# Optimization experiments

Measured on AMD Instinct MI355X. Metric: run time of the kernel, lower is better.

The kernel has to match this reference:

```python
import jax, jax.numpy as jnp
import numpy as np

# plan steps: (downsample_factor, bins_min, bins_max)
PLAN = [(2, 10, 14), (4, 16, 20)]


def _downsample(x, scale):
    # F.interpolate(mode='linear', align_corners=False, scale_factor=1/scale)
    in_len = x.shape[-1]
    out_len = in_len // scale
    sf = in_len / out_len
    src = jnp.maximum((jnp.arange(out_len, dtype=jnp.float32) + 0.5) * sf - 0.5, 0.0)
    i0 = jnp.floor(src).astype(jnp.int32)
    w = src - i0
    i1 = jnp.minimum(i0 + 1, in_len - 1)
    return x[..., i0] * (1.0 - w) + x[..., i1] * w


def _groupshiftadd(x, g):
    # one FFA butterfly stage with group size g
    B, C, R, nc = x.shape
    xg = x.reshape(B, C, R // g, g, nc)
    i = np.arange(g)
    iA = i // 2
    iB = iA + g // 2
    Bs = (i + 1) // 2
    # roll(v, Bs): y[j] = v[(j - Bs) mod nc]; static gather indices
    col = (np.arange(nc)[None, :] - Bs[:, None]) % nc  # (g, nc)
    a = xg[:, :, :, iA, :]                     # (B,C,G,g,nc)
    b = xg[:, :, :, iB[:, None], col]          # (B,C,G,g,nc) shifted rows
    return (a + b).reshape(B, C, R, nc)


def _forward(x):
    std_dev = jnp.std(x, axis=2, ddof=1)  # torch .std(2) is unbiased
    outs = []
    for ds, bmin, bmax in PLAN:
        down = _downsample(x, ds)
        L = down.shape[-1]
        for bins in range(bmin, bmax):
            trunc = L % bins
            arr = down[:, :, :L - trunc] if trunc else down
            r = arr.reshape(arr.shape[0], arr.shape[1], -1, bins)
            ini_rows = r.shape[2]
            k = int(np.ceil(np.log2(ini_rows)))
            target_rows = 2 ** k
            add = target_rows - ini_rows
            if add:
                pad = jnp.zeros((r.shape[0], r.shape[1], add, bins), r.dtype)
                r = jnp.concatenate([r, pad], axis=2)
            y = r
            for stage in range(1, k + 1):
                y = _groupshiftadd(y, 2 ** stage)
            mx = y.max(axis=3)
            # torch.median returns lower middle element for even sizes
            med = jnp.sort(y, axis=3)[..., (bins - 1) // 2]
            snr = (mx - med) / std_dev[:, :, None] / np.sqrt(float(ini_rows))
            outs.append(snr)  # (B, C, target_rows)
    return jnp.concatenate(outs, axis=2)


def setup_inputs() -> dict:
    key = jax.random.key(0)
    x = jax.random.normal(key, (8, 4, 262144), dtype=jnp.float32)
    return {"x": x}


def reference(x):
    return _forward(x)
```

## Files before the change

### kernel.cpp

```cpp
#include <hip/hip_runtime.h>
#include <cmath>


constexpr int NSEQ    = 32;
constexpr int NLEN    = 262144;
constexpr int OUTROWS = 81920;
constexpr int STDCH   = 32;

constexpr int cilog2(int v) { int r = 0; while (v > 1) { v >>= 1; ++r; } return r; }

constexpr size_t SCROFF[8] = {0, 6291456, 12582912, 18874368,
                              27262976, 29360128, 31981568, 34603008};

__device__ __forceinline__ unsigned bf16rne(float f) {
    unsigned u = __float_as_uint(f);
    return (u + 0x7FFFu + ((u >> 16) & 1u)) >> 16;
}
__device__ __forceinline__ unsigned pk2(float lo, float hi) {
    return bf16rne(lo) | (bf16rne(hi) << 16);
}

__global__ __launch_bounds__(256)
void std_partial(const float* __restrict__ x, float2* __restrict__ part)
{
    const int seq = blockIdx.x, ch = blockIdx.y;
    constexpr int N4 = NLEN / 4 / STDCH;
    const float4* xp = reinterpret_cast<const float4*>(x + (size_t)seq * NLEN) + (size_t)ch * N4;
    float s = 0.f, s2 = 0.f;
    for (int i = threadIdx.x; i < N4; i += 256) {
        float4 v = xp[i];
        s  += (v.x + v.y) + (v.z + v.w);
        s2 += (v.x * v.x + v.y * v.y) + (v.z * v.z + v.w * v.w);
    }
    #pragma unroll
    for (int off = 32; off > 0; off >>= 1) {
        s  += __shfl_down(s, off, 64);
        s2 += __shfl_down(s2, off, 64);
    }
    __shared__ float2 ws[4];
    const int w = threadIdx.x >> 6, l = threadIdx.x & 63;
    if (l == 0) ws[w] = make_float2(s, s2);
    __syncthreads();
    if (threadIdx.x == 0) {
        float a = ws[0].x + ws[1].x + ws[2].x + ws[3].x;
        float b = ws[0].y + ws[1].y + ws[2].y + ws[3].y;
        part[seq * STDCH + ch] = make_float2(a, b);
    }
}

template<int DS, int BINS, int K, int S0, int CPAD>
__device__ __forceinline__
void passA_body(float* __restrict__ buf, const float* __restrict__ xs,
                unsigned short* __restrict__ scrC, int R, int blk, int sl)
{
    constexpr int G      = 1 << S0;
    constexpr int M      = 1 << (K - S0);
    constexpr int PAIRS  = G / 2;
    constexpr int CSPLIT = 512 / PAIRS;
    constexpr int H      = (BINS + CSPLIT - 1) / CSPLIT;
    const int t = threadIdx.x;
    float* b0 = buf;
    float* b1 = buf + BINS * G;

    const int fmax = max(0, min(G * BINS, R * BINS - blk * G * BINS));

    if constexpr (DS == 2) {
        const float4* src4 = reinterpret_cast<const float4*>(xs + 2 * (size_t)blk * G * BINS);
        constexpr int NF4 = G * BINS / 2;
        for (int i = t; i < NF4; i += 512) {
            const int f0 = 2 * i;
            if (f0 < fmax) {
                float4 v = src4[i];
                int lr = f0 / BINS, c = f0 - lr * BINS;
                b0[c * G + lr] = 0.5f * (v.x + v.y);
                if (f0 + 1 < fmax) {
                    int c1 = c + 1, lr1 = lr;
                    if (c1 == BINS) { c1 = 0; ++lr1; }
                    b0[c1 * G + lr1] = 0.5f * (v.z + v.w);
                }
            }
        }
    } else {
        const float4* src4 = reinterpret_cast<const float4*>(xs + 4 * (size_t)blk * G * BINS);
        constexpr int NF4 = G * BINS;
        for (int i = t; i < NF4; i += 512) {
            if (i < fmax) {
                float4 v = src4[i];
                int lr = i / BINS, c = i - lr * BINS;
                b0[c * G + lr] = 0.5f * (v.y + v.z);
            }
        }
    }
    for (int f = fmax + t; f < G * BINS; f += 512) {
        int lr = f / BINS, c = f - lr * BINS;
        b0[c * G + lr] = 0.f;
    }
    __syncthreads();

    const int pr  = t & (PAIRS - 1);
    const int chi = t / PAIRS;
    const int c0  = chi * H;
    for (int s = 1; s <= S0; ++s) {
        const float* src = (s & 1) ? b0 : b1;
        float*       dst = (s & 1) ? b1 : b0;
        const int half    = 1 << (s - 1);
        const int qp      = pr & (half - 1);
        const int grpbase = (pr >> (s - 1)) << s;
        const int rA = grpbase + qp, rB = rA + half, ro = grpbase + 2 * qp;
        const int shift = qp % BINS;
        int sc = c0 - shift; if (sc < 0) sc += BINS;
        int scm1 = sc - 1;   if (scm1 < 0) scm1 += BINS;
        float bprev = src[scm1 * G + rB];
        #pragma unroll
        for (int i2 = 0; i2 < H; ++i2) {
            const int c = c0 + i2;
            if (c < BINS) {
                float a  = src[c * G + rA];
                float bc = src[sc * G + rB];
                float2 o; o.x = a + bc; o.y = a + bprev;
                *reinterpret_cast<float2*>(&dst[c * G + ro]) = o;
                bprev = bc;
                ++sc; if (sc == BINS) sc = 0;
            }
        }
        __syncthreads();
    }

    const float* fin = (S0 & 1) ? b1 : b0;
    if constexpr (G == 512) {
        const int lr = t;
        unsigned u[CPAD / 2];
        #pragma unroll
        for (int k = 0; k < CPAD / 2; ++k) {
            const int ca = 2 * k, cb = 2 * k + 1;
            float fa = (ca < BINS) ? fin[ca * G + lr] : 0.f;
            float fb = (cb < BINS) ? fin[cb * G + lr] : 0.f;
            u[k] = pk2(fa, fb);
        }
        unsigned short* dst = scrC + ((size_t)(sl * M + blk) * G + lr) * CPAD;
        if constexpr (CPAD == 12) {
            uint2* d2 = reinterpret_cast<uint2*>(dst);
            d2[0] = make_uint2(u[0], u[1]);
            d2[1] = make_uint2(u[2], u[3]);
            d2[2] = make_uint2(u[4], u[5]);
        } else {
            uint4* d4 = reinterpret_cast<uint4*>(dst);
            d4[0] = make_uint4(u[0], u[1], u[2], u[3]);
            d4[1] = make_uint4(u[4], u[5], u[6], u[7]);
        }
    } else {
        const int lr = t & 255, chh = t >> 8;
        constexpr int CH = CPAD / 2;
        unsigned u[CH / 2];
        #pragma unroll
        for (int k = 0; k < CH / 2; ++k) {
            const int ca = chh * CH + 2 * k, cb = ca + 1;
            float fa = (ca < BINS) ? fin[ca * G + lr] : 0.f;
            float fb = (cb < BINS) ? fin[cb * G + lr] : 0.f;
            u[k] = pk2(fa, fb);
        }
        unsigned short* dst = scrC + ((size_t)(sl * M + blk) * G + lr) * CPAD + chh * CH;
        if constexpr (CH == 8) {
            *reinterpret_cast<uint4*>(dst) = make_uint4(u[0], u[1], u[2], u[3]);
        } else {
            unsigned* d = reinterpret_cast<unsigned*>(dst);
            #pragma unroll
            for (int k = 0; k < CH / 2; ++k) d[k] = u[k];
        }
    }
}

__global__ __launch_bounds__(512, 6)
void passA_all(const float* __restrict__ x, unsigned short* __restrict__ scr)
{
    __shared__ float buf[2 * 13 * 512];
    const int b = blockIdx.x;
    if (b < 4096) {
        const int cfg = b >> 10, r = b & 1023, blk = r & 31, sl = r >> 5;
        const float* xs = x + (size_t)sl * NLEN;
        switch (cfg) {
            case 0: passA_body<2, 10, 14, 9, 12>(buf, xs, scr + SCROFF[0], 13107, blk, sl); break;
            case 1: passA_body<2, 11, 14, 9, 12>(buf, xs, scr + SCROFF[1], 11915, blk, sl); break;
            case 2: passA_body<2, 12, 14, 9, 12>(buf, xs, scr + SCROFF[2], 10922, blk, sl); break;
            default: passA_body<2, 13, 14, 9, 16>(buf, xs, scr + SCROFF[3], 10082, blk, sl); break;
        }
    } else {
        const int b2 = b - 4096;
        const int cfg = b2 >> 9, r = b2 & 511, blk = r & 15, sl = r >> 4;
        const float* xs = x + (size_t)sl * NLEN;
        switch (cfg) {
            case 0: passA_body<4, 16, 12, 8, 16>(buf, xs, scr + SCROFF[4], 4096, blk, sl); break;
            case 1: passA_body<4, 17, 12, 8, 20>(buf, xs, scr + SCROFF[5], 3855, blk, sl); break;
            case 2: passA_body<4, 18, 12, 8, 20>(buf, xs, scr + SCROFF[6], 3640, blk, sl); break;
            default: passA_body<4, 19, 12, 8, 20>(buf, xs, scr + SCROFF[7], 3449, blk, sl); break;
        }
    }
}

template<int BINS, int K, int S0, int CPAD, int OUTOFF>
__device__ __forceinline__
void passB_body(float* __restrict__ zb, float* __restrict__ s_red,
                const unsigned short* __restrict__ scrC, const float2* __restrict__ part,
                float* __restrict__ out, int R, int p_base, int sl)
{
    constexpr int G     = 1 << S0;
    constexpr int M     = 1 << (K - S0);
    constexpr int TS    = K - S0;
    constexpr int P     = 16;
    constexpr int CST   = M + 4;
    constexpr int BCST  = BINS * CST;
    constexpr int NCH   = 64 / M;
    constexpr int LNCH  = cilog2(NCH);
    constexpr int CEILB = (BINS + NCH - 1) / NCH;

    const int t = threadIdx.x;

    if (t < 64) {
        float s = 0.f, s2 = 0.f;
        if (t < 32) { float2 pp = part[sl * STDCH + t]; s = pp.x; s2 = pp.y; }
        #pragma unroll
        for (int off = 16; off > 0; off >>= 1) {
            s  += __shfl_down(s, off, 64);
            s2 += __shfl_down(s2, off, 64);
        }
        if (t == 0) {
            const float n = (float)NLEN;
            s_red[0] = rsqrtf((s2 - s * s / n) / (n - 1.f)) * rsqrtf((float)R);
        }
    }

    {
        constexpr int RUN = P * CPAD / 4;
        constexpr int TOT = M * RUN;
        const unsigned short* base = scrC + (size_t)sl * M * G * CPAD + (size_t)p_base * CPAD;
        for (int i = t; i < TOT; i += 512) {
            const int v = i / RUN, r = i - v * RUN;
            const uint2 d = *reinterpret_cast<const uint2*>(base + (size_t)v * G * CPAD + 4 * r);
            const int e0 = 4 * r;
            const int pl = e0 / CPAD, c = e0 - pl * CPAD;
            float* zp = zb + pl * BCST + v;
            if (c + 0 < BINS) zp[(c + 0) * CST] = __uint_as_float(d.x << 16);
            if (c + 1 < BINS) zp[(c + 1) * CST] = __uint_as_float(d.x & 0xFFFF0000u);
            if (c + 2 < BINS) zp[(c + 2) * CST] = __uint_as_float(d.y << 16);
            if (c + 3 < BINS) zp[(c + 3) * CST] = __uint_as_float(d.y & 0xFFFF0000u);
        }
    }
    __syncthreads();

    const int sub = t & 31, pg = t >> 5;
    const int p = p_base + pg;
    float* zpg = zb + pg * BCST;
    for (int s = 1; s <= TS; ++s) {
        const int half = 1 << (s - 1);
        const int q  = sub >> LNCH;
        const int ch = sub & (NCH - 1);
        const int qp = q & (half - 1);
        const int grp = (q >> (s - 1)) << s;
        const int vA = grp + qp, vB = vA + half, vo = grp + 2 * qp;
        const int shift = (qp + p * half) % BINS;
        float ra[CEILB], rb0[CEILB], rb1[CEILB];
        #pragma unroll
        for (int i2 = 0; i2 < CEILB; ++i2) {
            const int c = ch + i2 * NCH;
            if (c < BINS) {
                int sc0 = c - shift; if (sc0 < 0) sc0 += BINS;
                int sc1 = sc0 - 1;   if (sc1 < 0) sc1 += BINS;
                ra[i2]  = zpg[c   * CST + vA];
                rb0[i2] = zpg[sc0 * CST + vB];
                rb1[i2] = zpg[sc1 * CST + vB];
            }
        }
        __syncthreads();
        #pragma unroll
        for (int i2 = 0; i2 < CEILB; ++i2) {
            const int c = ch + i2 * NCH;
            if (c < BINS) {
                float2 o; o.x = ra[i2] + rb0[i2]; o.y = ra[i2] + rb1[i2];
                *reinterpret_cast<float2*>(&zpg[c * CST + vo]) = o;
            }
        }
        __syncthreads();
    }

    constexpr int ROWS = P * M;
    if (t < ROWS) {
        const int pg2 = t >> TS;
        const int v   = t & (M - 1);
        const float* z = zb + pg2 * BCST;
        float a[BINS];
        #pragma unroll
        for (int c = 0; c < BINS; ++c) a[c] = z[c * CST + v];
        float mx = a[0];
        #pragma unroll
        for (int c = 1; c < BINS; ++c) mx = fmaxf(mx, a[c]);
        constexpr int MIDX = (BINS - 1) / 2;
        #pragma unroll
        for (int i = 0; i <= MIDX; ++i) {
            #pragma unroll
            for (int j = i + 1; j < BINS; ++j) {
                float lo = fminf(a[i], a[j]);
                float hi = fmaxf(a[i], a[j]);
                a[i] = lo; a[j] = hi;
            }
        }
        out[(size_t)sl * OUTROWS + OUTOFF + (size_t)p_base * M + t] = (mx - a[MIDX]) * s_red[0];
    }
}

__global__ __launch_bounds__(512, 6)
void passB_all(const unsigned short* __restrict__ scr, const float2* __restrict__ part,
               float* __restrict__ out)
{
    __shared__ float zb[16 * 13 * 36];
    __shared__ float s_red[1];
    const int b = blockIdx.x;
    if (b < 4096) {
        const int cfg = b >> 10, r = b & 1023, pb = r & 31, sl = r >> 5;
        const int p_base = pb * 16;
        switch (cfg) {
            case 0: passB_body<10, 14, 9, 12, 0>    (zb, s_red, scr + SCROFF[0], part, out, 13107, p_base, sl); break;
            case 1: passB_body<11, 14, 9, 12, 16384>(zb, s_red, scr + SCROFF[1], part, out, 11915, p_base, sl); break;
            case 2: passB_body<12, 14, 9, 12, 32768>(zb, s_red, scr + SCROFF[2], part, out, 10922, p_base, sl); break;
            default: passB_body<13, 14, 9, 16, 49152>(zb, s_red, scr + SCROFF[3], part, out, 10082, p_base, sl); break;
        }
    } else {
        const int b2 = b - 4096;
        const int cfg = b2 >> 9, r = b2 & 511, pb = r & 15, sl = r >> 4;
        const int p_base = pb * 16;
        switch (cfg) {
            case 0: passB_body<16, 12, 8, 16, 65536>(zb, s_red, scr + SCROFF[4], part, out, 4096, p_base, sl); break;
            case 1: passB_body<17, 12, 8, 20, 69632>(zb, s_red, scr + SCROFF[5], part, out, 3855, p_base, sl); break;
            case 2: passB_body<18, 12, 8, 20, 73728>(zb, s_red, scr + SCROFF[6], part, out, 3640, p_base, sl); break;
            default: passB_body<19, 12, 8, 20, 77824>(zb, s_red, scr + SCROFF[7], part, out, 3449, p_base, sl); break;
        }
    }
}

extern "C" void kernel_launch(void* const* d_in, const int* in_sizes, int n_in,
                              void* d_out, int out_size, void* d_ws, size_t ws_size,
                              hipStream_t stream)
{
    (void)in_sizes; (void)n_in; (void)out_size; (void)ws_size;
    const float* x = (const float*)d_in[0];
    float* out  = (float*)d_out;
    float* wsf  = (float*)d_ws;
    float2* part = reinterpret_cast<float2*>(wsf + 64);
    unsigned short* scr = reinterpret_cast<unsigned short*>(wsf + 2176);

    hipLaunchKernelGGL(std_partial, dim3(NSEQ, STDCH), dim3(256), 0, stream, x, part);
    hipLaunchKernelGGL(passA_all, dim3(6144), dim3(512), 0, stream, x, scr);
    hipLaunchKernelGGL(passB_all, dim3(6144), dim3(512), 0, stream, scr, part, out);
}
```

Baseline: 165.0 us.

## Fuse pairs of FFA butterfly stages into radix-4 passes in shared memory

Replaces the per-stage butterfly loops in both pass A and pass B with fused two-stage kernels that read four rows and write float4 outputs, halving the number of shared-memory round trips and __syncthreads barriers. The odd leftover stage is handled by a single-stage helper. The cost is more live registers, more complex shift/index arithmetic, and the stage count is now hardcoded (S0 of 8 or 9, TS of 4 or 5), so other configurations would break.

```diff
diff --git a/kernel.cpp b/kernel.cpp
--- a/kernel.cpp
+++ b/kernel.cpp
@@ -11,6 +11,9 @@
 
 constexpr size_t SCROFF[8] = {0, 6291456, 12582912, 18874368,
                               27262976, 29360128, 31981568, 34603008};
+
+template<int B>
+__device__ __forceinline__ int mb(int x) { return ((x % B) + B) % B; }
 
 __device__ __forceinline__ unsigned bf16rne(float f) {
     unsigned u = __float_as_uint(f);
@@ -48,6 +51,109 @@
     }
 }
 
+template<int BINS, int G, int H, int LQ>
+__device__ __forceinline__
+void fusedA(const float* __restrict__ src, float* __restrict__ dst, int s)
+{
+    constexpr int QUADS = G / 4;
+    const int t = threadIdx.x;
+    const int Q   = t & (QUADS - 1);
+    const int chi = t >> LQ;
+    const int c0  = chi * H;
+    const int h = 1 << (s - 1), S = 1 << s;
+    const int q  = Q & (h - 1);
+    const int G2 = (Q >> (s - 1)) << (s + 1);
+    const int rA0 = G2 + q, rA1 = rA0 + h, rB0 = G2 + S + q, rB1 = rB0 + h;
+    const int vo = G2 + 4 * q;
+    int ca = mb<BINS>(c0 - q), ga = mb<BINS>(c0 - 2 * q), cb = mb<BINS>(c0 - 3 * q);
+    float a1p  = src[mb<BINS>(c0 - q - 1) * G + rA1];
+    float b1p  = src[mb<BINS>(c0 - 3 * q - 1) * G + rB1];
+    float b0m1 = src[mb<BINS>(c0 - 2 * q - 1) * G + rB0];
+    float b0m2 = src[mb<BINS>(c0 - 2 * q - 2) * G + rB0];
+    float b1m2 = src[mb<BINS>(c0 - 3 * q - 2) * G + rB1];
+    float b1m3 = src[mb<BINS>(c0 - 3 * q - 3) * G + rB1];
+    float v0p = b0m1 + b1p, v1p = b0m1 + b1m2, v1pp = b0m2 + b1m3;
+    #pragma unroll
+    for (int i2 = 0; i2 < H; ++i2) {
+        const int c = c0 + i2;
+        if (c < BINS) {
+            float a0 = src[c * G + rA0];
+            float a1 = src[ca * G + rA1];
+            float b0 = src[ga * G + rB0];
+            float b1 = src[cb * G + rB1];
+            float u0 = a0 + a1, u1 = a0 + a1p;
+            float v0 = b0 + b1, v1 = b0 + b1p;
+            float4 o; o.x = u0 + v0; o.y = u0 + v0p; o.z = u1 + v1p; o.w = u1 + v1pp;
+            *reinterpret_cast<float4*>(&dst[c * G + vo]) = o;
+            a1p = a1; b1p = b1; v1pp = v1p; v1p = v1; v0p = v0;
+            ++ca; if (ca == BINS) ca = 0;
+            ++ga; if (ga == BINS) ga = 0;
+            ++cb; if (cb == BINS) cb = 0;
+        }
+    }
+}
+
+template<int BINS, int G, int H, int LQ>
+__device__ __forceinline__
+void fusedA1(const float* __restrict__ src, float* __restrict__ dst)
+{
+    constexpr int QUADS = G / 4;
+    const int t = threadIdx.x;
+    const int Q   = t & (QUADS - 1);
+    const int chi = t >> LQ;
+    const int c0  = chi * H;
+    const int r4  = 4 * Q;
+    float4 fm1 = *reinterpret_cast<const float4*>(&src[mb<BINS>(c0 - 1) * G + r4]);
+    float4 fm2 = *reinterpret_cast<const float4*>(&src[mb<BINS>(c0 - 2) * G + r4]);
+    float4 fm3 = *reinterpret_cast<const float4*>(&src[mb<BINS>(c0 - 3) * G + r4]);
+    float a1p = fm1.y, b1p = fm1.w;
+    float v0p  = fm1.z + fm1.w;
+    float v1p  = fm1.z + fm2.w;
+    float v1pp = fm2.z + fm3.w;
+    #pragma unroll
+    for (int i2 = 0; i2 < H; ++i2) {
+        const int c = c0 + i2;
+        if (c < BINS) {
+            float4 f = *reinterpret_cast<const float4*>(&src[c * G + r4]);
+            float u0 = f.x + f.y, u1 = f.x + a1p;
+            float v0 = f.z + f.w, v1 = f.z + b1p;
+            float4 o; o.x = u0 + v0; o.y = u0 + v0p; o.z = u1 + v1p; o.w = u1 + v1pp;
+            *reinterpret_cast<float4*>(&dst[c * G + r4]) = o;
+            a1p = f.y; b1p = f.w; v1pp = v1p; v1p = v1; v0p = v0;
+        }
+    }
+}
+
+template<int BINS, int G, int H1, int LP>
+__device__ __forceinline__
+void singleA(const float* __restrict__ src, float* __restrict__ dst, int s)
+{
+    constexpr int PAIRS = G / 2;
+    const int t = threadIdx.x;
+    const int pr  = t & (PAIRS - 1);
+    const int chi = t >> LP;
+    const int c0  = chi * H1;
+    const int half = 1 << (s - 1);
+    const int qp = pr & (half - 1);
+    const int grpbase = (pr >> (s - 1)) << s;
+    const int rA = grpbase + qp, rB = rA + half, ro = grpbase + 2 * qp;
+    const int shift = qp % BINS;
+    int sc = mb<BINS>(c0 - shift);
+    float bprev = src[mb<BINS>(c0 - shift - 1) * G + rB];
+    #pragma unroll
+    for (int i2 = 0; i2 < H1; ++i2) {
+        const int c = c0 + i2;
+        if (c < BINS) {
+            float a  = src[c * G + rA];
+            float bc = src[sc * G + rB];
+            float2 o; o.x = a + bc; o.y = a + bprev;
+            *reinterpret_cast<float2*>(&dst[c * G + ro]) = o;
+            bprev = bc;
+            ++sc; if (sc == BINS) sc = 0;
+        }
+    }
+}
+
 template<int DS, int BINS, int K, int S0, int CPAD>
 __device__ __forceinline__
 void passA_body(float* __restrict__ buf, const float* __restrict__ xs,
@@ -55,9 +161,14 @@
 {
     constexpr int G      = 1 << S0;
     constexpr int M      = 1 << (K - S0);
+    constexpr int QUADS  = G / 4;
+    constexpr int LQ     = cilog2(QUADS);
+    constexpr int CSPLIT = 512 / QUADS;
+    constexpr int H      = (BINS + CSPLIT - 1) / CSPLIT;
     constexpr int PAIRS  = G / 2;
-    constexpr int CSPLIT = 512 / PAIRS;
-    constexpr int H      = (BINS + CSPLIT - 1) / CSPLIT;
+    constexpr int LP     = cilog2(PAIRS);
+    constexpr int CS1    = 512 / PAIRS;
+    constexpr int H1     = (BINS + CS1 - 1) / CS1;
     const int t = threadIdx.x;
     float* b0 = buf;
     float* b1 = buf + BINS * G;
@@ -97,33 +208,12 @@
     }
     __syncthreads();
 
-    const int pr  = t & (PAIRS - 1);
-    const int chi = t / PAIRS;
-    const int c0  = chi * H;
-    for (int s = 1; s <= S0; ++s) {
-        const float* src = (s & 1) ? b0 : b1;
-        float*       dst = (s & 1) ? b1 : b0;
-        const int half    = 1 << (s - 1);
-        const int qp      = pr & (half - 1);
-        const int grpbase = (pr >> (s - 1)) << s;
-        const int rA = grpbase + qp, rB = rA + half, ro = grpbase + 2 * qp;
-        const int shift = qp % BINS;
-        int sc = c0 - shift; if (sc < 0) sc += BINS;
-        int scm1 = sc - 1;   if (scm1 < 0) scm1 += BINS;
-        float bprev = src[scm1 * G + rB];
-        #pragma unroll
-        for (int i2 = 0; i2 < H; ++i2) {
-            const int c = c0 + i2;
-            if (c < BINS) {
-                float a  = src[c * G + rA];
-                float bc = src[sc * G + rB];
-                float2 o; o.x = a + bc; o.y = a + bprev;
-                *reinterpret_cast<float2*>(&dst[c * G + ro]) = o;
-                bprev = bc;
-                ++sc; if (sc == BINS) sc = 0;
-            }
-        }
-        __syncthreads();
+    fusedA1<BINS, G, H, LQ>(b0, b1);    __syncthreads();
+    fusedA <BINS, G, H, LQ>(b1, b0, 3); __syncthreads();
+    fusedA <BINS, G, H, LQ>(b0, b1, 5); __syncthreads();
+    fusedA <BINS, G, H, LQ>(b1, b0, 7); __syncthreads();
+    if constexpr (S0 == 9) {
+        singleA<BINS, G, H1, LP>(b0, b1, 9); __syncthreads();
     }
 
     const float* fin = (S0 & 1) ? b1 : b0;
@@ -132,9 +222,9 @@
         unsigned u[CPAD / 2];
         #pragma unroll
         for (int k = 0; k < CPAD / 2; ++k) {
-            const int ca = 2 * k, cb = 2 * k + 1;
-            float fa = (ca < BINS) ? fin[ca * G + lr] : 0.f;
-            float fb = (cb < BINS) ? fin[cb * G + lr] : 0.f;
+            const int ca = 2 * k, cbn = 2 * k + 1;
+            float fa = (ca < BINS)  ? fin[ca * G + lr]  : 0.f;
+            float fb = (cbn < BINS) ? fin[cbn * G + lr] : 0.f;
             u[k] = pk2(fa, fb);
         }
         unsigned short* dst = scrC + ((size_t)(sl * M + blk) * G + lr) * CPAD;
@@ -154,9 +244,9 @@
         unsigned u[CH / 2];
         #pragma unroll
         for (int k = 0; k < CH / 2; ++k) {
-            const int ca = chh * CH + 2 * k, cb = ca + 1;
-            float fa = (ca < BINS) ? fin[ca * G + lr] : 0.f;
-            float fb = (cb < BINS) ? fin[cb * G + lr] : 0.f;
+            const int ca = chh * CH + 2 * k, cbn = ca + 1;
+            float fa = (ca < BINS)  ? fin[ca * G + lr]  : 0.f;
+            float fb = (cbn < BINS) ? fin[cbn * G + lr] : 0.f;
             u[k] = pk2(fa, fb);
         }
         unsigned short* dst = scrC + ((size_t)(sl * M + blk) * G + lr) * CPAD + chh * CH;
@@ -197,21 +287,121 @@
     }
 }
 
+template<int BINS, int M, int CST, int HB, int LQ>
+__device__ __forceinline__
+void fusedB(float* __restrict__ zpg, int s, int p, int sub)
+{
+    constexpr int QUADS = M / 4;
+    const int Q   = sub & (QUADS - 1);
+    const int chi = sub >> LQ;
+    const int c0  = chi * HB;
+    const int h = 1 << (s - 1), S = 1 << s;
+    const int q  = Q & (h - 1);
+    const int G2 = (Q >> (s - 1)) << (s + 1);
+    const int rA0 = G2 + q, rA1 = rA0 + h, rB0 = G2 + S + q, rB1 = rB0 + h;
+    const int vo = G2 + 4 * q;
+    const int ba1 = mb<BINS>(c0 - q - p * h - 1);
+    const int bb0 = mb<BINS>(c0 - 2 * q - p * S - 2);
+    const int bb1 = mb<BINS>(c0 - 3 * q - p * (S + h) - 3);
+
+    float fa0[HB], fa1[HB + 1], fb0[HB + 2], fb1[HB + 3];
+    #pragma unroll
+    for (int i = 0; i < HB; ++i) {
+        int cc = c0 + i; if (cc >= BINS) cc = BINS - 1;
+        fa0[i] = zpg[cc * CST + rA0];
+    }
+    int idx = ba1;
+    #pragma unroll
+    for (int i = 0; i < HB + 1; ++i) {
+        fa1[i] = zpg[idx * CST + rA1];
+        ++idx; if (idx == BINS) idx = 0;
+    }
+    idx = bb0;
+    #pragma unroll
+    for (int i = 0; i < HB + 2; ++i) {
+        fb0[i] = zpg[idx * CST + rB0];
+        ++idx; if (idx == BINS) idx = 0;
+    }
+    idx = bb1;
+    #pragma unroll
+    for (int i = 0; i < HB + 3; ++i) {
+        fb1[i] = zpg[idx * CST + rB1];
+        ++idx; if (idx == BINS) idx = 0;
+    }
+    __syncthreads();
+    #pragma unroll
+    for (int i2 = 0; i2 < HB; ++i2) {
+        const int c = c0 + i2;
+        if (c < BINS) {
+            float u0 = fa0[i2] + fa1[i2 + 1];
+            float u1 = fa0[i2] + fa1[i2];
+            float v0c  = fb0[i2 + 2] + fb1[i2 + 3];
+            float v0p  = fb0[i2 + 1] + fb1[i2 + 2];
+            float v1p  = fb0[i2 + 1] + fb1[i2 + 1];
+            float v1pp = fb0[i2]     + fb1[i2];
+            float4 o; o.x = u0 + v0c; o.y = u0 + v0p; o.z = u1 + v1p; o.w = u1 + v1pp;
+            *reinterpret_cast<float4*>(&zpg[c * CST + vo]) = o;
+        }
+    }
+    __syncthreads();
+}
+
+template<int BINS, int M, int CST, int HSB, int LP>
+__device__ __forceinline__
+void singleB(float* __restrict__ zpg, int s, int p, int sub)
+{
+    constexpr int PAIRSB = M / 2;
+    const int pr  = sub & (PAIRSB - 1);
+    const int chi = sub >> LP;
+    const int c0  = chi * HSB;
+    const int half = 1 << (s - 1);
+    const int qp = pr & (half - 1);
+    const int grpbase = (pr >> (s - 1)) << s;
+    const int rA = grpbase + qp, rB = rA + half, ro = grpbase + 2 * qp;
+    const int shift = (qp + p * half) % BINS;
+
+    float ra[HSB], rb[HSB + 1];
+    #pragma unroll
+    for (int i = 0; i < HSB; ++i) {
+        int cc = c0 + i; if (cc >= BINS) cc = BINS - 1;
+        ra[i] = zpg[cc * CST + rA];
+    }
+    int idx = mb<BINS>(c0 - shift - 1);
+    #pragma unroll
+    for (int i = 0; i < HSB + 1; ++i) {
+        rb[i] = zpg[idx * CST + rB];
+        ++idx; if (idx == BINS) idx = 0;
+    }
+    __syncthreads();
+    #pragma unroll
+    for (int i2 = 0; i2 < HSB; ++i2) {
+        const int c = c0 + i2;
+        if (c < BINS) {
+            float2 o; o.x = ra[i2] + rb[i2 + 1]; o.y = ra[i2] + rb[i2];
+            *reinterpret_cast<float2*>(&zpg[c * CST + ro]) = o;
+        }
+    }
+    __syncthreads();
+}
+
 template<int BINS, int K, int S0, int CPAD, int OUTOFF>
 __device__ __forceinline__
 void passB_body(float* __restrict__ zb, float* __restrict__ s_red,
                 const unsigned short* __restrict__ scrC, const float2* __restrict__ part,
                 float* __restrict__ out, int R, int p_base, int sl)
 {
-    constexpr int G     = 1 << S0;
-    constexpr int M     = 1 << (K - S0);
-    constexpr int TS    = K - S0;
-    constexpr int P     = 16;
-    constexpr int CST   = M + 4;
-    constexpr int BCST  = BINS * CST;
-    constexpr int NCH   = 64 / M;
-    constexpr int LNCH  = cilog2(NCH);
-    constexpr int CEILB = (BINS + NCH - 1) / NCH;
+    constexpr int G    = 1 << S0;
+    constexpr int M    = 1 << (K - S0);
+    constexpr int TS   = K - S0;
+    constexpr int P    = 16;
+    constexpr int CST  = M + 4;
+    constexpr int BCST = BINS * CST;
+    constexpr int LQB  = cilog2(M / 4);
+    constexpr int CHB  = 32 / (M / 4);
+    constexpr int HB   = (BINS + CHB - 1) / CHB;
+    constexpr int LPB  = cilog2(M / 2);
+    constexpr int CSB  = 32 / (M / 2);
+    constexpr int HSB  = (BINS + CSB - 1) / CSB;
 
     const int t = threadIdx.x;
 
@@ -250,36 +440,10 @@
     const int sub = t & 31, pg = t >> 5;
     const int p = p_base + pg;
     float* zpg = zb + pg * BCST;
-    for (int s = 1; s <= TS; ++s) {
-        const int half = 1 << (s - 1);
-        const int q  = sub >> LNCH;
-        const int ch = sub & (NCH - 1);
-        const int qp = q & (half - 1);
-        const int grp = (q >> (s - 1)) << s;
-        const int vA = grp + qp, vB = vA + half, vo = grp + 2 * qp;
-        const int shift = (qp + p * half) % BINS;
-        float ra[CEILB], rb0[CEILB], rb1[CEILB];
-        #pragma unroll
-        for (int i2 = 0; i2 < CEILB; ++i2) {
-            const int c = ch + i2 * NCH;
-            if (c < BINS) {
-                int sc0 = c - shift; if (sc0 < 0) sc0 += BINS;
-                int sc1 = sc0 - 1;   if (sc1 < 0) sc1 += BINS;
-                ra[i2]  = zpg[c   * CST + vA];
-                rb0[i2] = zpg[sc0 * CST + vB];
-                rb1[i2] = zpg[sc1 * CST + vB];
-            }
-        }
-        __syncthreads();
-        #pragma unroll
-        for (int i2 = 0; i2 < CEILB; ++i2) {
-            const int c = ch + i2 * NCH;
-            if (c < BINS) {
-                float2 o; o.x = ra[i2] + rb0[i2]; o.y = ra[i2] + rb1[i2];
-                *reinterpret_cast<float2*>(&zpg[c * CST + vo]) = o;
-            }
-        }
-        __syncthreads();
+    fusedB<BINS, M, CST, HB, LQB>(zpg, 1, p, sub);
+    fusedB<BINS, M, CST, HB, LQB>(zpg, 3, p, sub);
+    if constexpr (TS == 5) {
+        singleB<BINS, M, CST, HSB, LPB>(zpg, 5, p, sub);
     }
 
     constexpr int ROWS = P * M;
```

Measured after the change: 162.7 us. Within noise of the previous version (-1.4%).
